# Performance work log

Measured on AMD Instinct MI355X. Metric: run time of the kernel, lower is better.

The kernel has to match this reference:

```python
import jax, jax.numpy as jnp
import numpy as np

SIZE = (2, 2)


def setup_inputs() -> dict:
    key = jax.random.key(0)
    k1, k2 = jax.random.split(key)
    B, H, W, C = 16, 64, 64, 128
    out_size = B * H * SIZE[0] * W * SIZE[1] * C  # 33_554_432
    updates = jax.random.normal(k1, (B, H, W, C), dtype=jnp.float32)
    mask = jax.random.randint(k2, (B, H, W, C), 0, out_size, dtype=jnp.int32)
    return {"updates": updates, "mask": mask}


def reference(updates, mask):
    # MaxUnpooling2D: scatter flattened updates into a zero buffer of the
    # full (upsampled) output size using flattened argmax indices, then reshape.
    B, H, W, C = updates.shape
    out_h, out_w = H * SIZE[0], W * SIZE[1]
    out_size = B * out_h * out_w * C
    # tf.scatter_nd sums duplicate indices -> use .add (matches semantics)
    flat = jnp.zeros((out_size,), dtype=updates.dtype).at[mask.reshape(-1)].add(
        updates.reshape(-1)
    )
    return flat.reshape(B, out_h, out_w, C)
```

## Files before the change

### kernel.cpp

```cpp
#include <hip/hip_runtime.h>


#define NB        2048
#define NB_SHIFT  14
#define RB        16384
#define P1B       1024
#define IPB       8192

__global__ __launch_bounds__(256) void partition_kernel(
        const float4* __restrict__ upd4,
        const int4*   __restrict__ mask4,
        unsigned int* __restrict__ tableA,
        uint2*        __restrict__ pairs) {
    __shared__ unsigned int hb[NB];
    __shared__ unsigned int tsum[256];
    __shared__ uint2 stage[IPB];
    const int t = threadIdx.x;
    const int k = blockIdx.x;
    const int s4 = k * (IPB / 4);

    for (int b = t; b < NB; b += 256) hb[b] = 0u;
    __syncthreads();

    int4 mm[IPB / 4 / 256];
    #pragma unroll
    for (int j = 0; j < IPB / 4 / 256; ++j) mm[j] = mask4[s4 + j * 256 + t];
    #pragma unroll
    for (int j = 0; j < IPB / 4 / 256; ++j) {
        atomicAdd(&hb[((unsigned)mm[j].x) >> NB_SHIFT], 1u);
        atomicAdd(&hb[((unsigned)mm[j].y) >> NB_SHIFT], 1u);
        atomicAdd(&hb[((unsigned)mm[j].z) >> NB_SHIFT], 1u);
        atomicAdd(&hb[((unsigned)mm[j].w) >> NB_SHIFT], 1u);
    }
    __syncthreads();

    unsigned c[8], s = 0;
    #pragma unroll
    for (int j = 0; j < 8; ++j) { c[j] = hb[t * 8 + j]; s += c[j]; }
    tsum[t] = s;
    __syncthreads();
    #pragma unroll
    for (int d = 1; d < 256; d <<= 1) {
        unsigned v = (t >= d) ? tsum[t - d] : 0u;
        __syncthreads();
        tsum[t] += v;
        __syncthreads();
    }
    unsigned run = (t > 0) ? tsum[t - 1] : 0u;
    #pragma unroll
    for (int j = 0; j < 8; ++j) {
        unsigned b = t * 8 + j;
        hb[b] = run;
        tableA[(size_t)k * NB + b] = run | (c[j] << 16);
        run += c[j];
    }
    __syncthreads();

    float4 uu[IPB / 4 / 256];
    #pragma unroll
    for (int j = 0; j < IPB / 4 / 256; ++j) uu[j] = upd4[s4 + j * 256 + t];
    #pragma unroll
    for (int j = 0; j < IPB / 4 / 256; ++j) {
        #define PLACE(mi, vi) { \
            unsigned b_ = ((unsigned)(mi)) >> NB_SHIFT; \
            unsigned pos_ = atomicAdd(&hb[b_], 1u); \
            stage[pos_] = make_uint2(((unsigned)(mi)) & (RB - 1u), __float_as_uint(vi)); }
        PLACE(mm[j].x, uu[j].x)
        PLACE(mm[j].y, uu[j].y)
        PLACE(mm[j].z, uu[j].z)
        PLACE(mm[j].w, uu[j].w)
        #undef PLACE
    }
    __syncthreads();

    const uint4* sp = (const uint4*)stage;
    uint4* dp = (uint4*)(pairs + (size_t)k * IPB);
    #pragma unroll
    for (int j = 0; j < IPB / 2 / 256; ++j) dp[j * 256 + t] = sp[j * 256 + t];
}

__global__ __launch_bounds__(256) void transpose_kernel(
        const unsigned int* __restrict__ A, unsigned int* __restrict__ B) {
    __shared__ unsigned int tile[32][33];
    const int tx = threadIdx.x & 31, ty = threadIdx.x >> 5;
    const int bx = blockIdx.x;
    const int by = blockIdx.y;
    #pragma unroll
    for (int r = 0; r < 32; r += 8)
        tile[ty + r][tx] = A[(size_t)(by * 32 + ty + r) * NB + bx * 32 + tx];
    __syncthreads();
    #pragma unroll
    for (int r = 0; r < 32; r += 8)
        B[(size_t)(bx * 32 + ty + r) * P1B + by * 32 + tx] = tile[tx][ty + r];
}

__global__ __launch_bounds__(256) void unbin_kernel(
        const unsigned int* __restrict__ tableB,
        const uint2*        __restrict__ pairs,
        float4*             __restrict__ out4) {
    extern __shared__ float tile[];
    __shared__ unsigned choff[P1B];
    __shared__ unsigned chbase[P1B];
    __shared__ unsigned wpart[4];
    __shared__ unsigned Ttot;
    const int b = blockIdx.x, t = threadIdx.x;
    float4* t4 = (float4*)tile;

    for (int j = t; j < RB / 4; j += 256) t4[j] = make_float4(0.f, 0.f, 0.f, 0.f);

    uint4 e = ((const uint4*)(tableB + (size_t)b * P1B))[t];
    unsigned c0 = e.x >> 16, c1 = e.y >> 16, c2 = e.z >> 16, c3 = e.w >> 16;
    unsigned s = c0 + c1 + c2 + c3;

    unsigned inc = s;
    #pragma unroll
    for (int d = 1; d < 64; d <<= 1) {
        unsigned v = __shfl_up(inc, d, 64);
        if ((t & 63) >= d) inc += v;
    }
    if ((t & 63) == 63) wpart[t >> 6] = inc;
    __syncthreads();
    unsigned wbase = 0;
    #pragma unroll
    for (int w = 0; w < 4; ++w) if (w < (t >> 6)) wbase += wpart[w];
    unsigned ex = wbase + inc - s;

    const unsigned k0 = t * 4;
    choff[k0 + 0] = ex;                 chbase[k0 + 0] = (k0 + 0) * IPB + (e.x & 0xFFFFu);
    choff[k0 + 1] = ex + c0;            chbase[k0 + 1] = (k0 + 1) * IPB + (e.y & 0xFFFFu);
    choff[k0 + 2] = ex + c0 + c1;       chbase[k0 + 2] = (k0 + 2) * IPB + (e.z & 0xFFFFu);
    choff[k0 + 3] = ex + c0 + c1 + c2;  chbase[k0 + 3] = (k0 + 3) * IPB + (e.w & 0xFFFFu);
    if (t == 255) Ttot = ex + s;
    __syncthreads();

    const unsigned T = Ttot;
    for (unsigned i = t; i < T; i += 256) {
        unsigned k = 0;
        #pragma unroll
        for (unsigned stp = 512; stp; stp >>= 1) {
            unsigned nk = k + stp;
            if (nk < P1B && choff[nk] <= i) k = nk;
        }
        uint2 pr = pairs[chbase[k] + (i - choff[k])];
        atomicAdd(&tile[pr.x], __uint_as_float(pr.y));
    }
    __syncthreads();

    for (int j = t; j < RB / 4; j += 256)
        out4[(size_t)b * (RB / 4) + j] = t4[j];
}

__global__ void zero_out_kernel(float4* __restrict__ out, int n4) {
    int i = blockIdx.x * blockDim.x + threadIdx.x;
    if (i < n4) out[i] = make_float4(0.f, 0.f, 0.f, 0.f);
}
__global__ void scatter_add_kernel(const float4* __restrict__ upd,
                                   const int4* __restrict__ mask,
                                   float* __restrict__ out, int n4) {
    int i = blockIdx.x * blockDim.x + threadIdx.x;
    if (i < n4) {
        float4 u = upd[i];
        int4 m = mask[i];
        atomicAdd(out + m.x, u.x);
        atomicAdd(out + m.y, u.y);
        atomicAdd(out + m.z, u.z);
        atomicAdd(out + m.w, u.w);
    }
}

extern "C" void kernel_launch(void* const* d_in, const int* in_sizes, int n_in,
                              void* d_out, int out_size, void* d_ws, size_t ws_size,
                              hipStream_t stream) {
    const float* updates = (const float*)d_in[0];
    const int*   mask    = (const int*)d_in[1];
    float* out = (float*)d_out;
    const int n  = in_sizes[0];
    const int n4 = n >> 2;
    const int o4 = out_size >> 2;

    const size_t pairs_b  = (size_t)P1B * IPB * sizeof(uint2);
    const size_t table_b  = (size_t)P1B * NB * sizeof(unsigned);
    const size_t need = pairs_b + 2 * table_b;
    if (ws_size >= need && out_size == NB * RB && n == P1B * IPB) {
        uint2* pairs = (uint2*)d_ws;
        unsigned* tableA = (unsigned*)((char*)d_ws + pairs_b);
        unsigned* tableB = (unsigned*)((char*)d_ws + pairs_b + table_b);

        partition_kernel<<<P1B, 256, 0, stream>>>(
            (const float4*)updates, (const int4*)mask, tableA, pairs);
        transpose_kernel<<<dim3(NB / 32, P1B / 32), 256, 0, stream>>>(tableA, tableB);
        unbin_kernel<<<NB, 256, RB * sizeof(float), stream>>>(
            tableB, pairs, (float4*)out);
    } else {
        zero_out_kernel<<<(o4 + 255) / 256, 256, 0, stream>>>((float4*)out, o4);
        scatter_add_kernel<<<(n4 + 255) / 256, 256, 0, stream>>>(
            (const float4*)updates, (const int4*)mask, out, n4);
    }
}
```

Before: 298.4 us.

## Walk bin chunks per thread with 16-byte loads instead of binary-search flattening

```diff
diff --git a/kernel.cpp b/kernel.cpp
--- a/kernel.cpp
+++ b/kernel.cpp
@@ -98,51 +98,49 @@
         const unsigned int* __restrict__ tableB,
         const uint2*        __restrict__ pairs,
         float4*             __restrict__ out4) {
-    extern __shared__ float tile[];
-    __shared__ unsigned choff[P1B];
-    __shared__ unsigned chbase[P1B];
-    __shared__ unsigned wpart[4];
-    __shared__ unsigned Ttot;
-    const int b = blockIdx.x, t = threadIdx.x;
+    __shared__ float tile[RB];
+    const int t = threadIdx.x;
+    const int b = ((blockIdx.x & 7) << 8) | (blockIdx.x >> 3);
     float4* t4 = (float4*)tile;
 
     for (int j = t; j < RB / 4; j += 256) t4[j] = make_float4(0.f, 0.f, 0.f, 0.f);
 
     uint4 e = ((const uint4*)(tableB + (size_t)b * P1B))[t];
-    unsigned c0 = e.x >> 16, c1 = e.y >> 16, c2 = e.z >> 16, c3 = e.w >> 16;
-    unsigned s = c0 + c1 + c2 + c3;
-
-    unsigned inc = s;
-    #pragma unroll
-    for (int d = 1; d < 64; d <<= 1) {
-        unsigned v = __shfl_up(inc, d, 64);
-        if ((t & 63) >= d) inc += v;
-    }
-    if ((t & 63) == 63) wpart[t >> 6] = inc;
-    __syncthreads();
-    unsigned wbase = 0;
-    #pragma unroll
-    for (int w = 0; w < 4; ++w) if (w < (t >> 6)) wbase += wpart[w];
-    unsigned ex = wbase + inc - s;
-
-    const unsigned k0 = t * 4;
-    choff[k0 + 0] = ex;                 chbase[k0 + 0] = (k0 + 0) * IPB + (e.x & 0xFFFFu);
-    choff[k0 + 1] = ex + c0;            chbase[k0 + 1] = (k0 + 1) * IPB + (e.y & 0xFFFFu);
-    choff[k0 + 2] = ex + c0 + c1;       chbase[k0 + 2] = (k0 + 2) * IPB + (e.z & 0xFFFFu);
-    choff[k0 + 3] = ex + c0 + c1 + c2;  chbase[k0 + 3] = (k0 + 3) * IPB + (e.w & 0xFFFFu);
-    if (t == 255) Ttot = ex + s;
+    unsigned s0 = (unsigned)(t * 4 + 0) * IPB + (e.x & 0xFFFFu), e0 = s0 + (e.x >> 16);
+    unsigned s1 = (unsigned)(t * 4 + 1) * IPB + (e.y & 0xFFFFu), e1 = s1 + (e.y >> 16);
+    unsigned s2 = (unsigned)(t * 4 + 2) * IPB + (e.z & 0xFFFFu), e2 = s2 + (e.z >> 16);
+    unsigned s3 = (unsigned)(t * 4 + 3) * IPB + (e.w & 0xFFFFu), e3 = s3 + (e.w >> 16);
+    unsigned a0 = s0 & ~1u, a1 = s1 & ~1u, a2 = s2 & ~1u, a3 = s3 & ~1u;
     __syncthreads();
 
-    const unsigned T = Ttot;
-    for (unsigned i = t; i < T; i += 256) {
-        unsigned k = 0;
-        #pragma unroll
-        for (unsigned stp = 512; stp; stp >>= 1) {
-            unsigned nk = k + stp;
-            if (nk < P1B && choff[nk] <= i) k = nk;
+    const uint4* p4 = (const uint4*)pairs;
+    while ((a0 < e0) | (a1 < e1) | (a2 < e2) | (a3 < e3)) {
+        bool c0 = a0 < e0, c1 = a1 < e1, c2 = a2 < e2, c3 = a3 < e3;
+        uint4 v0, v1, v2, v3;
+        if (c0) v0 = p4[a0 >> 1];
+        if (c1) v1 = p4[a1 >> 1];
+        if (c2) v2 = p4[a2 >> 1];
+        if (c3) v3 = p4[a3 >> 1];
+        if (c0) {
+            if (a0 >= s0)     atomicAdd(&tile[v0.x], __uint_as_float(v0.y));
+            if (a0 + 1 < e0)  atomicAdd(&tile[v0.z], __uint_as_float(v0.w));
+            a0 += 2;
         }
-        uint2 pr = pairs[chbase[k] + (i - choff[k])];
-        atomicAdd(&tile[pr.x], __uint_as_float(pr.y));
+        if (c1) {
+            if (a1 >= s1)     atomicAdd(&tile[v1.x], __uint_as_float(v1.y));
+            if (a1 + 1 < e1)  atomicAdd(&tile[v1.z], __uint_as_float(v1.w));
+            a1 += 2;
+        }
+        if (c2) {
+            if (a2 >= s2)     atomicAdd(&tile[v2.x], __uint_as_float(v2.y));
+            if (a2 + 1 < e2)  atomicAdd(&tile[v2.z], __uint_as_float(v2.w));
+            a2 += 2;
+        }
+        if (c3) {
+            if (a3 >= s3)     atomicAdd(&tile[v3.x], __uint_as_float(v3.y));
+            if (a3 + 1 < e3)  atomicAdd(&tile[v3.z], __uint_as_float(v3.w));
+            a3 += 2;
+        }
     }
     __syncthreads();
 
@@ -189,8 +187,7 @@
         partition_kernel<<<P1B, 256, 0, stream>>>(
             (const float4*)updates, (const int4*)mask, tableA, pairs);
         transpose_kernel<<<dim3(NB / 32, P1B / 32), 256, 0, stream>>>(tableA, tableB);
-        unbin_kernel<<<NB, 256, RB * sizeof(float), stream>>>(
-            tableB, pairs, (float4*)out);
+        unbin_kernel<<<NB, 256, 0, stream>>>(tableB, pairs, (float4*)out);
     } else {
         zero_out_kernel<<<(o4 + 255) / 256, 256, 0, stream>>>((float4*)out, o4);
         scatter_add_kernel<<<(n4 + 255) / 256, 256, 0, stream>>>(
```

Result: faster. 256.9 us (-13.9%).
